# Kernel tuning notes

Hardware: AMD Instinct MI355X
Metric: run time of the kernel (lower is better)

## Reference

```python
import jax, jax.numpy as jnp
import numpy as np

N = 100000
E = 1600000
NFEAT, NHID1, NHID2, NCLASS, NSTRUC = 512, 256, 128, 40, 128


def glorot(key, shape):
    lim = 1.0 / np.sqrt(shape[0])
    return jax.random.uniform(key, shape, jnp.float32, -lim, lim)


def setup_inputs() -> dict:
    key = jax.random.key(0)
    ks = jax.random.split(key, 12)
    x = jax.random.normal(ks[0], (N, NFEAT), jnp.float32)
    edge_index = jax.random.randint(ks[1], (2, E), 0, N, jnp.int32)
    edge_weight = jax.random.uniform(ks[2], (E,), jnp.float32)
    return {
        "x": x,
        "edge_index": edge_index,
        "edge_weight": edge_weight,
        "W1": glorot(ks[3], (NFEAT, NHID1)), "b1": jnp.zeros((NHID1,), jnp.float32),
        "W2": glorot(ks[4], (NHID1, NHID2)), "b2": jnp.zeros((NHID2,), jnp.float32),
        "W3": glorot(ks[5], (NHID2, NCLASS)), "b3": jnp.zeros((NCLASS,), jnp.float32),
        "We": glorot(ks[6], (NHID1, NSTRUC)), "be": jnp.zeros((NSTRUC,), jnp.float32),
    }


def spmm(edge_index, edge_weight, support):
    # adj @ support with adj given as weighted edge list (dst <- src)
    src, dst = edge_index[0], edge_index[1]
    msgs = support[src] * edge_weight[:, None]  # [E, d]
    return jax.ops.segment_sum(msgs, dst, num_segments=N)


def gc_layer(x, edge_index, edge_weight, W, b):
    support = x @ W
    return spmm(edge_index, edge_weight, support) + b


def reference(x, edge_index, edge_weight, W1, b1, W2, b2, W3, b3, We, be):
    # eval mode: dropout is identity
    h = jax.nn.relu(gc_layer(x, edge_index, edge_weight, W1, b1))
    out1 = jax.nn.relu(gc_layer(h, edge_index, edge_weight, W2, b2))
    out1 = gc_layer(out1, edge_index, edge_weight, W3, b3)
    out2 = h @ We + be
    return jax.nn.log_softmax(out1, axis=1), out2
```

## Files before the change

kernel.cpp:

```cpp
#include <hip/hip_runtime.h>
#include <hip/hip_bf16.h>

#define NNODES 100000
#define NEDGES 1600000

typedef __attribute__((ext_vector_type(8))) short bf16x8;
typedef __attribute__((ext_vector_type(4))) short bf16x4;
typedef __attribute__((ext_vector_type(2))) short bf16x2;
typedef __attribute__((ext_vector_type(4))) float f32x4;
typedef __attribute__((ext_vector_type(2))) float f32x2;

static __device__ __forceinline__ short f2bf(float f) {
  __hip_bfloat16 b = __float2bfloat16(f);
  return __builtin_bit_cast(short, b);
}
static __device__ __forceinline__ float bf2f(short s) {
  unsigned int u = ((unsigned int)(unsigned short)s) << 16;
  return __builtin_bit_cast(float, u);
}
static __device__ __forceinline__ void fma4(f32x4& a, float w, bf16x4 v) {
  a[0] = fmaf(w, bf2f(v[0]), a[0]);
  a[1] = fmaf(w, bf2f(v[1]), a[1]);
  a[2] = fmaf(w, bf2f(v[2]), a[2]);
  a[3] = fmaf(w, bf2f(v[3]), a[3]);
}
static __device__ __forceinline__ void fma2(f32x2& a, float w, bf16x2 v) {
  a[0] = fmaf(w, bf2f(v[0]), a[0]);
  a[1] = fmaf(w, bf2f(v[1]), a[1]);
}

__global__ void wtrans_kernel(const float* __restrict__ W, short* __restrict__ Wt,
                              int K, int Nvalid, int Npad) {
  int idx = blockIdx.x * blockDim.x + threadIdx.x;
  if (idx >= Npad * K) return;
  int n = idx / K, k = idx - n * K;
  Wt[idx] = (n < Nvalid) ? f2bf(W[(size_t)k * Nvalid + n]) : (short)0;
}

__global__ void hist_kernel(const int* __restrict__ ei, int* __restrict__ deg) {
  int e = blockIdx.x * blockDim.x + threadIdx.x;
  if (e < NEDGES) atomicAdd(&deg[ei[NEDGES + e]], 1);
}

__global__ void scan1_kernel(const int* __restrict__ deg, int* __restrict__ out,
                             int* __restrict__ bsums) {
  __shared__ int lds[256];
  int tid = threadIdx.x;
  int base = blockIdx.x * 1024 + tid * 4;
  int v[4];
#pragma unroll
  for (int j = 0; j < 4; j++) v[j] = (base + j < NNODES) ? deg[base + j] : 0;
  int s = v[0] + v[1] + v[2] + v[3];
  lds[tid] = s;
  __syncthreads();
  for (int off = 1; off < 256; off <<= 1) {
    int t = (tid >= off) ? lds[tid - off] : 0;
    __syncthreads();
    lds[tid] += t;
    __syncthreads();
  }
  int incl = lds[tid];
  if (tid == 255) bsums[blockIdx.x] = incl;
  int run = incl - s;
#pragma unroll
  for (int j = 0; j < 4; j++) {
    if (base + j < NNODES) out[base + j] = run;
    run += v[j];
  }
}

__global__ void scan2_kernel(const int* __restrict__ bsums, int* __restrict__ bex, int nb) {
  __shared__ int lds[128];
  int tid = threadIdx.x;
  int s = (tid < nb) ? bsums[tid] : 0;
  lds[tid] = s;
  __syncthreads();
  for (int off = 1; off < 128; off <<= 1) {
    int t = (tid >= off) ? lds[tid - off] : 0;
    __syncthreads();
    lds[tid] += t;
    __syncthreads();
  }
  if (tid < nb) bex[tid] = lds[tid] - s;
}

__global__ void scan3_kernel(int* __restrict__ rowptr, int* __restrict__ cursor,
                             const int* __restrict__ bex) {
  int i = blockIdx.x * blockDim.x + threadIdx.x;
  if (i < NNODES) {
    int v = rowptr[i] + bex[i >> 10];
    rowptr[i] = v;
    cursor[i] = v;
  }
  if (i == 0) rowptr[NNODES] = NEDGES;
}

__global__ void scatter_kernel(const int* __restrict__ ei, const float* __restrict__ ew,
                               int* __restrict__ cursor, int2* __restrict__ edat) {
  int e = blockIdx.x * blockDim.x + threadIdx.x;
  if (e >= NEDGES) return;
  int s = ei[e], d = ei[NEDGES + e];
  int p = atomicAdd(&cursor[d], 1);
  edat[p] = make_int2(s, __float_as_int(ew[e]));
}

#define LDSTR 72
template <bool AF32, int EPI>
__launch_bounds__(256, 2)
__global__ void gemm_tiled(const void* __restrict__ Aptr, int K,
                           const short* __restrict__ Wt,
                           void* __restrict__ Cp0, float* __restrict__ Cp1,
                           const float* __restrict__ bias, int nvalid, int ldc) {
  __shared__ __align__(16) short As[128 * LDSTR];
  __shared__ __align__(16) short Bs[128 * LDSTR];
  int tid = threadIdx.x;
  int lane = tid & 63, wv = tid >> 6;
  int wr = wv >> 1, wc = wv & 1;
  int m0 = blockIdx.x * 128;
  int n0 = blockIdx.y * 128;
  f32x4 acc[4][4];
#pragma unroll
  for (int i = 0; i < 4; i++)
#pragma unroll
    for (int j = 0; j < 4; j++) acc[i][j] = (f32x4){0.f, 0.f, 0.f, 0.f};

  int srow = tid >> 3;
  int scol = (tid & 7) * 8;

  for (int k0 = 0; k0 < K; k0 += 64) {
#pragma unroll
    for (int p = 0; p < 4; p++) {
      int ml = p * 32 + srow;
      int arow = m0 + ml;
      if (arow >= NNODES) arow = NNODES - 1;
      bf16x8 av;
      if (AF32) {
        const float* ap = (const float*)Aptr + (size_t)arow * K + k0 + scol;
        f32x4 a0 = *(const f32x4*)ap;
        f32x4 a1 = *(const f32x4*)(ap + 4);
#pragma unroll
        for (int j = 0; j < 4; j++) { av[j] = f2bf(a0[j]); av[4 + j] = f2bf(a1[j]); }
      } else {
        av = *(const bf16x8*)((const short*)Aptr + (size_t)arow * K + k0 + scol);
      }
      *(bf16x8*)&As[ml * LDSTR + scol] = av;
      bf16x8 bv = *(const bf16x8*)(Wt + (size_t)(n0 + ml) * K + k0 + scol);
      *(bf16x8*)&Bs[ml * LDSTR + scol] = bv;
    }
    __syncthreads();
    int r = lane & 15, quad = lane >> 4;
#pragma unroll
    for (int kk = 0; kk < 64; kk += 32) {
      bf16x8 af[4], bfr[4];
#pragma unroll
      for (int i = 0; i < 4; i++)
        af[i] = *(const bf16x8*)&As[(wr * 64 + i * 16 + r) * LDSTR + kk + quad * 8];
#pragma unroll
      for (int j = 0; j < 4; j++)
        bfr[j] = *(const bf16x8*)&Bs[(wc * 64 + j * 16 + r) * LDSTR + kk + quad * 8];
#pragma unroll
      for (int i = 0; i < 4; i++)
#pragma unroll
        for (int j = 0; j < 4; j++)
          acc[i][j] = __builtin_amdgcn_mfma_f32_16x16x32_bf16(af[i], bfr[j], acc[i][j], 0, 0, 0);
    }
    __syncthreads();
  }

  int quad = lane >> 4, cl = lane & 15;
#pragma unroll
  for (int i = 0; i < 4; i++) {
    int rowb = m0 + wr * 64 + i * 16 + quad * 4;
#pragma unroll
    for (int rr = 0; rr < 4; rr++) {
      int row = rowb + rr;
      if (row < NNODES) {
#pragma unroll
        for (int j = 0; j < 4; j++) {
          int col = n0 + wc * 64 + j * 16 + cl;
          float v = acc[i][j][rr];
          if (EPI == 0) {
            ((short*)Cp0)[(size_t)row * ldc + col] = f2bf(v);
          } else if (EPI == 1) {
            if (col < nvalid) Cp1[(size_t)row * nvalid + col] = v;
          } else {
            if (col < 128) ((short*)Cp0)[(size_t)row * 128 + col] = f2bf(v);
            else Cp1[(size_t)row * 128 + (col - 128)] = v + bias[col - 128];
          }
        }
      }
    }
  }
}

__global__ void spmm1_kernel(const int* __restrict__ rowptr, const int2* __restrict__ edat,
                             const short* __restrict__ S,
                             const float* __restrict__ bias, short* __restrict__ H) {
  int node = blockIdx.x * 4 + (threadIdx.x >> 6);
  if (node >= NNODES) return;
  int lane = threadIdx.x & 63;
  int c0 = lane * 4;
  const short* Sc = S + c0;
  f32x4 acc0 = (f32x4){0.f, 0.f, 0.f, 0.f};
  f32x4 acc1 = (f32x4){0.f, 0.f, 0.f, 0.f};
  int beg = rowptr[node], end = rowptr[node + 1];
  int i = beg;
  for (; i + 8 <= end; i += 8) {
    int2 e[8];
    bf16x4 v[8];
#pragma unroll
    for (int j = 0; j < 8; j++) e[j] = edat[i + j];
#pragma unroll
    for (int j = 0; j < 8; j++) v[j] = *(const bf16x4*)(Sc + (size_t)e[j].x * 256);
#pragma unroll
    for (int j = 0; j < 8; j++) {
      float w = __int_as_float(e[j].y);
      if (j & 1) fma4(acc1, w, v[j]); else fma4(acc0, w, v[j]);
    }
  }
  for (; i < end; i++) {
    int2 e = edat[i];
    fma4(acc0, __int_as_float(e.y), *(const bf16x4*)(Sc + (size_t)e.x * 256));
  }
  f32x4 a;
  a[0] = acc0[0] + acc1[0]; a[1] = acc0[1] + acc1[1];
  a[2] = acc0[2] + acc1[2]; a[3] = acc0[3] + acc1[3];
  f32x4 b = *(const f32x4*)(bias + c0);
  bf16x4 h;
#pragma unroll
  for (int j = 0; j < 4; j++) h[j] = f2bf(fmaxf(a[j] + b[j], 0.f));
  *(bf16x4*)(H + (size_t)node * 256 + c0) = h;
}

__global__ void spmm2_kernel(const int* __restrict__ rowptr, const int2* __restrict__ edat,
                             const short* __restrict__ S,
                             const float* __restrict__ bias, short* __restrict__ H) {
  int node = blockIdx.x * 4 + (threadIdx.x >> 6);
  if (node >= NNODES) return;
  int lane = threadIdx.x & 63;
  int c0 = lane * 2;
  const short* Sc = S + c0;
  f32x2 acc0 = (f32x2){0.f, 0.f};
  f32x2 acc1 = (f32x2){0.f, 0.f};
  int beg = rowptr[node], end = rowptr[node + 1];
  int i = beg;
  for (; i + 8 <= end; i += 8) {
    int2 e[8];
    bf16x2 v[8];
#pragma unroll
    for (int j = 0; j < 8; j++) e[j] = edat[i + j];
#pragma unroll
    for (int j = 0; j < 8; j++) v[j] = *(const bf16x2*)(Sc + (size_t)e[j].x * 128);
#pragma unroll
    for (int j = 0; j < 8; j++) {
      float w = __int_as_float(e[j].y);
      if (j & 1) fma2(acc1, w, v[j]); else fma2(acc0, w, v[j]);
    }
  }
  for (; i < end; i++) {
    int2 e = edat[i];
    fma2(acc0, __int_as_float(e.y), *(const bf16x2*)(Sc + (size_t)e.x * 128));
  }
  float a0 = acc0[0] + acc1[0], a1 = acc0[1] + acc1[1];
  bf16x2 h;
  h[0] = f2bf(fmaxf(a0 + bias[c0 + 0], 0.f));
  h[1] = f2bf(fmaxf(a1 + bias[c0 + 1], 0.f));
  *(bf16x2*)(H + (size_t)node * 128 + c0) = h;
}

__global__ void spmm3_kernel(const int* __restrict__ rowptr, const int2* __restrict__ edat,
                             const float* __restrict__ S3,
                             const float* __restrict__ b3, float* __restrict__ out1) {
  int node = blockIdx.x * 4 + (threadIdx.x >> 6);
  if (node >= NNODES) return;
  int lane = threadIdx.x & 63;
  bool act = lane < 40;
  float acc0 = 0.f, acc1 = 0.f;
  int beg = rowptr[node], end = rowptr[node + 1];
  if (act) {
    int i = beg;
    for (; i + 8 <= end; i += 8) {
      int2 e[8];
      float v[8];
#pragma unroll
      for (int j = 0; j < 8; j++) e[j] = edat[i + j];
#pragma unroll
      for (int j = 0; j < 8; j++) v[j] = S3[(size_t)e[j].x * 40 + lane];
#pragma unroll
      for (int j = 0; j < 8; j++) {
        float w = __int_as_float(e[j].y);
        if (j & 1) acc1 = fmaf(w, v[j], acc1); else acc0 = fmaf(w, v[j], acc0);
      }
    }
    for (; i < end; i++) {
      int2 e = edat[i];
      acc0 = fmaf(__int_as_float(e.y), S3[(size_t)e.x * 40 + lane], acc0);
    }
  }
  float acc = acc0 + acc1;
  if (act) acc += b3[lane];
  float v = act ? acc : -__builtin_inff();
  for (int off = 32; off > 0; off >>= 1) v = fmaxf(v, __shfl_xor(v, off));
  float e = act ? expf(acc - v) : 0.f;
  for (int off = 32; off > 0; off >>= 1) e += __shfl_xor(e, off);
  float ls = logf(e);
  if (act) out1[(size_t)node * 40 + lane] = acc - v - ls;
}

extern "C" void kernel_launch(void* const* d_in, const int* in_sizes, int n_in,
                              void* d_out, int out_size, void* d_ws, size_t ws_size,
                              hipStream_t stream) {
  const float* x  = (const float*)d_in[0];
  const int*   ei = (const int*)d_in[1];
  const float* ew = (const float*)d_in[2];
  const float* W1 = (const float*)d_in[3];
  const float* b1 = (const float*)d_in[4];
  const float* W2 = (const float*)d_in[5];
  const float* b2 = (const float*)d_in[6];
  const float* W3 = (const float*)d_in[7];
  const float* b3 = (const float*)d_in[8];
  const float* We = (const float*)d_in[9];
  const float* be = (const float*)d_in[10];
  float* out1 = (float*)d_out;
  float* out2 = (float*)d_out + (size_t)NNODES * 40;

  char* w = (char*)d_ws;
  size_t off = 0;
  auto alloc = [&](size_t bytes) -> char* {
    char* p = w + off;
    off += (bytes + 255) & ~(size_t)255;
    return p;
  };
  int*   deg    = (int*)alloc((size_t)NNODES * 4);
  int*   rowptr = (int*)alloc((size_t)(NNODES + 1) * 4);
  int*   cursor = (int*)alloc((size_t)NNODES * 4);
  int*   bsums  = (int*)alloc(512);
  int*   bex    = (int*)alloc(512);
  int2*  edat   = (int2*)alloc((size_t)NEDGES * 8);
  short* Wt1    = (short*)alloc((size_t)256 * 512 * 2);
  short* Wt2e   = (short*)alloc((size_t)256 * 256 * 2);
  short* Wt3    = (short*)alloc((size_t)128 * 128 * 2);
  short* S1bf   = (short*)alloc((size_t)NNODES * 256 * 2);
  short* Hbf    = (short*)alloc((size_t)NNODES * 256 * 2);
  short* S2bf   = (short*)alloc((size_t)NNODES * 128 * 2);
  short* Tbf    = (short*)alloc((size_t)NNODES * 128 * 2);
  float* S3     = (float*)alloc((size_t)NNODES * 40 * 4);

  hipMemsetAsync(deg, 0, (size_t)NNODES * 4, stream);
  hist_kernel<<<(NEDGES + 255) / 256, 256, 0, stream>>>(ei, deg);
  int nb = (NNODES + 1023) / 1024;
  scan1_kernel<<<nb, 256, 0, stream>>>(deg, rowptr, bsums);
  scan2_kernel<<<1, 128, 0, stream>>>(bsums, bex, nb);
  scan3_kernel<<<(NNODES + 255) / 256, 256, 0, stream>>>(rowptr, cursor, bex);
  scatter_kernel<<<(NEDGES + 255) / 256, 256, 0, stream>>>(ei, ew, cursor, edat);

  wtrans_kernel<<<(256 * 512 + 255) / 256, 256, 0, stream>>>(W1, Wt1, 512, 256, 256);
  wtrans_kernel<<<(128 * 256 + 255) / 256, 256, 0, stream>>>(W2, Wt2e, 256, 128, 128);
  wtrans_kernel<<<(128 * 256 + 255) / 256, 256, 0, stream>>>(We, Wt2e + (size_t)128 * 256, 256, 128, 128);
  wtrans_kernel<<<(128 * 128 + 255) / 256, 256, 0, stream>>>(W3, Wt3, 128, 40, 128);

  int gblocks = (NNODES + 127) / 128;
  int sblocks = (NNODES + 3) / 4;

  gemm_tiled<true, 0><<<dim3(gblocks, 2), 256, 0, stream>>>(x, 512, Wt1, S1bf, nullptr, nullptr, 256, 256);
  spmm1_kernel<<<sblocks, 256, 0, stream>>>(rowptr, edat, S1bf, b1, Hbf);
  gemm_tiled<false, 2><<<dim3(gblocks, 2), 256, 0, stream>>>(Hbf, 256, Wt2e, S2bf, out2, be, 256, 128);
  spmm2_kernel<<<sblocks, 256, 0, stream>>>(rowptr, edat, S2bf, b2, Tbf);
  gemm_tiled<false, 1><<<dim3(gblocks, 1), 256, 0, stream>>>(Tbf, 128, Wt3, nullptr, S3, nullptr, 40, 40);
  spmm3_kernel<<<sblocks, 256, 0, stream>>>(rowptr, edat, S3, b3, out1);
}
```

Baseline: 884.5 us.

## Build CSR via two-level bucket sort and swap GEMM grid axes

Replaces the per-node histogram, three-kernel scan and atomic scatter with a two-pass bucketed counting sort. Edges are first grouped into 128-node buckets using LDS histograms, then each bucket is sorted locally in LDS, which writes rowptr and edat. This cuts global atomics and should make the edge writes closer to coalesced. It packs the local destination into the high bits of the source index, which assumes node ids fit in 17 bits, and reuses the S3 buffer as scratch. Separately, the GEMM grid axes are swapped so the N-tiles of one M-row block run next to each other, which should improve L2 reuse of the A rows.

```diff
diff --git a/kernel.cpp b/kernel.cpp
--- a/kernel.cpp
+++ b/kernel.cpp
@@ -3,6 +3,8 @@
 
 #define NNODES 100000
 #define NEDGES 1600000
+#define BSH 7
+#define NBUCK ((NNODES + 127) >> 7)
 
 typedef __attribute__((ext_vector_type(8))) short bf16x8;
 typedef __attribute__((ext_vector_type(4))) short bf16x4;
@@ -37,71 +39,99 @@
   Wt[idx] = (n < Nvalid) ? f2bf(W[(size_t)k * Nvalid + n]) : (short)0;
 }
 
-__global__ void hist_kernel(const int* __restrict__ ei, int* __restrict__ deg) {
-  int e = blockIdx.x * blockDim.x + threadIdx.x;
-  if (e < NEDGES) atomicAdd(&deg[ei[NEDGES + e]], 1);
-}
-
-__global__ void scan1_kernel(const int* __restrict__ deg, int* __restrict__ out,
-                             int* __restrict__ bsums) {
-  __shared__ int lds[256];
+__global__ void bcount_kernel(const int* __restrict__ ei, int* __restrict__ bcnt) {
+  __shared__ int h[NBUCK];
+  for (int i = threadIdx.x; i < NBUCK; i += 256) h[i] = 0;
+  __syncthreads();
+  int stride = gridDim.x * 256;
+  for (int e = blockIdx.x * 256 + threadIdx.x; e < NEDGES; e += stride)
+    atomicAdd(&h[ei[NEDGES + e] >> BSH], 1);
+  __syncthreads();
+  for (int i = threadIdx.x; i < NBUCK; i += 256)
+    if (h[i]) atomicAdd(&bcnt[i], h[i]);
+}
+
+__global__ void bscan_kernel(const int* __restrict__ bcnt, int* __restrict__ bbase,
+                             int* __restrict__ bcur, int* __restrict__ rowptr) {
+  __shared__ int lds[1024];
+  int t = threadIdx.x;
+  int c = (t < NBUCK) ? bcnt[t] : 0;
+  lds[t] = c;
+  __syncthreads();
+  for (int off = 1; off < 1024; off <<= 1) {
+    int v = (t >= off) ? lds[t - off] : 0;
+    __syncthreads();
+    lds[t] += v;
+    __syncthreads();
+  }
+  if (t < NBUCK) {
+    int ex = lds[t] - c;
+    bbase[t] = ex;
+    bcur[t] = ex;
+  }
+  if (t == NBUCK) bbase[t] = NEDGES;
+  if (t == 0) rowptr[NNODES] = NEDGES;
+}
+
+#define P4CHUNK 8192
+__global__ void bscatter_kernel(const int* __restrict__ ei, const float* __restrict__ ew,
+                                int* __restrict__ bcur, int2* __restrict__ tmp) {
+  __shared__ int cnt[NBUCK];
+  __shared__ int pos[NBUCK];
   int tid = threadIdx.x;
-  int base = blockIdx.x * 1024 + tid * 4;
-  int v[4];
-#pragma unroll
-  for (int j = 0; j < 4; j++) v[j] = (base + j < NNODES) ? deg[base + j] : 0;
-  int s = v[0] + v[1] + v[2] + v[3];
-  lds[tid] = s;
-  __syncthreads();
-  for (int off = 1; off < 256; off <<= 1) {
-    int t = (tid >= off) ? lds[tid - off] : 0;
-    __syncthreads();
-    lds[tid] += t;
-    __syncthreads();
-  }
-  int incl = lds[tid];
-  if (tid == 255) bsums[blockIdx.x] = incl;
-  int run = incl - s;
-#pragma unroll
-  for (int j = 0; j < 4; j++) {
-    if (base + j < NNODES) out[base + j] = run;
-    run += v[j];
-  }
-}
-
-__global__ void scan2_kernel(const int* __restrict__ bsums, int* __restrict__ bex, int nb) {
-  __shared__ int lds[128];
+  for (int i = tid; i < NBUCK; i += 256) cnt[i] = 0;
+  __syncthreads();
+  int base = blockIdx.x * P4CHUNK;
+  int end = base + P4CHUNK;
+  if (end > NEDGES) end = NEDGES;
+  for (int e = base + tid; e < end; e += 256)
+    atomicAdd(&cnt[ei[NEDGES + e] >> BSH], 1);
+  __syncthreads();
+  for (int i = tid; i < NBUCK; i += 256)
+    if (cnt[i]) pos[i] = atomicAdd(&bcur[i], cnt[i]);
+  __syncthreads();
+  for (int e = base + tid; e < end; e += 256) {
+    int d = ei[NEDGES + e];
+    int b = d >> BSH;
+    int p = atomicAdd(&pos[b], 1);
+    tmp[p] = make_int2(ei[e] | ((d & 127) << 17), __float_as_int(ew[e]));
+  }
+}
+
+__global__ void bsort_kernel(const int* __restrict__ bbase, const int2* __restrict__ tmp,
+                             int2* __restrict__ edat, int* __restrict__ rowptr) {
+  __shared__ int hist[128];
+  __shared__ int cur[128];
+  int b = blockIdx.x;
   int tid = threadIdx.x;
-  int s = (tid < nb) ? bsums[tid] : 0;
-  lds[tid] = s;
+  int base = bbase[b], cnt = bbase[b + 1] - base;
+  if (tid < 128) hist[tid] = 0;
+  __syncthreads();
+  for (int i = tid; i < cnt; i += 256)
+    atomicAdd(&hist[(tmp[base + i].x >> 17) & 127], 1);
+  __syncthreads();
+  int c = (tid < 128) ? hist[tid] : 0;
+  if (tid < 128) cur[tid] = c;
   __syncthreads();
   for (int off = 1; off < 128; off <<= 1) {
-    int t = (tid >= off) ? lds[tid - off] : 0;
-    __syncthreads();
-    lds[tid] += t;
-    __syncthreads();
-  }
-  if (tid < nb) bex[tid] = lds[tid] - s;
-}
-
-__global__ void scan3_kernel(int* __restrict__ rowptr, int* __restrict__ cursor,
-                             const int* __restrict__ bex) {
-  int i = blockIdx.x * blockDim.x + threadIdx.x;
-  if (i < NNODES) {
-    int v = rowptr[i] + bex[i >> 10];
-    rowptr[i] = v;
-    cursor[i] = v;
-  }
-  if (i == 0) rowptr[NNODES] = NEDGES;
-}
-
-__global__ void scatter_kernel(const int* __restrict__ ei, const float* __restrict__ ew,
-                               int* __restrict__ cursor, int2* __restrict__ edat) {
-  int e = blockIdx.x * blockDim.x + threadIdx.x;
-  if (e >= NEDGES) return;
-  int s = ei[e], d = ei[NEDGES + e];
-  int p = atomicAdd(&cursor[d], 1);
-  edat[p] = make_int2(s, __float_as_int(ew[e]));
+    int v = (tid < 128 && tid >= off) ? cur[tid - off] : 0;
+    __syncthreads();
+    if (tid < 128) cur[tid] += v;
+    __syncthreads();
+  }
+  if (tid < 128) {
+    int ex = cur[tid] - c;
+    int node = (b << BSH) + tid;
+    if (node < NNODES) rowptr[node] = base + ex;
+    cur[tid] = base + ex;
+  }
+  __syncthreads();
+  for (int i = tid; i < cnt; i += 256) {
+    int2 r = tmp[base + i];
+    int d = (r.x >> 17) & 127;
+    int p = atomicAdd(&cur[d], 1);
+    edat[p] = make_int2(r.x & 0x1FFFF, r.y);
+  }
 }
 
 #define LDSTR 72
@@ -116,8 +146,8 @@
   int tid = threadIdx.x;
   int lane = tid & 63, wv = tid >> 6;
   int wr = wv >> 1, wc = wv & 1;
-  int m0 = blockIdx.x * 128;
-  int n0 = blockIdx.y * 128;
+  int m0 = blockIdx.y * 128;
+  int n0 = blockIdx.x * 128;
   f32x4 acc[4][4];
 #pragma unroll
   for (int i = 0; i < 4; i++)
@@ -331,11 +361,10 @@
     off += (bytes + 255) & ~(size_t)255;
     return p;
   };
-  int*   deg    = (int*)alloc((size_t)NNODES * 4);
   int*   rowptr = (int*)alloc((size_t)(NNODES + 1) * 4);
-  int*   cursor = (int*)alloc((size_t)NNODES * 4);
-  int*   bsums  = (int*)alloc(512);
-  int*   bex    = (int*)alloc(512);
+  int*   bcnt   = (int*)alloc((size_t)NBUCK * 4);
+  int*   bbase  = (int*)alloc((size_t)(NBUCK + 1) * 4);
+  int*   bcur   = (int*)alloc((size_t)NBUCK * 4);
   int2*  edat   = (int2*)alloc((size_t)NEDGES * 8);
   short* Wt1    = (short*)alloc((size_t)256 * 512 * 2);
   short* Wt2e   = (short*)alloc((size_t)256 * 256 * 2);
@@ -345,14 +374,13 @@
   short* S2bf   = (short*)alloc((size_t)NNODES * 128 * 2);
   short* Tbf    = (short*)alloc((size_t)NNODES * 128 * 2);
   float* S3     = (float*)alloc((size_t)NNODES * 40 * 4);
-
-  hipMemsetAsync(deg, 0, (size_t)NNODES * 4, stream);
-  hist_kernel<<<(NEDGES + 255) / 256, 256, 0, stream>>>(ei, deg);
-  int nb = (NNODES + 1023) / 1024;
-  scan1_kernel<<<nb, 256, 0, stream>>>(deg, rowptr, bsums);
-  scan2_kernel<<<1, 128, 0, stream>>>(bsums, bex, nb);
-  scan3_kernel<<<(NNODES + 255) / 256, 256, 0, stream>>>(rowptr, cursor, bex);
-  scatter_kernel<<<(NEDGES + 255) / 256, 256, 0, stream>>>(ei, ew, cursor, edat);
+  int2*  tmp    = (int2*)S3;
+
+  hipMemsetAsync(bcnt, 0, (size_t)NBUCK * 4, stream);
+  bcount_kernel<<<256, 256, 0, stream>>>(ei, bcnt);
+  bscan_kernel<<<1, 1024, 0, stream>>>(bcnt, bbase, bcur, rowptr);
+  bscatter_kernel<<<(NEDGES + P4CHUNK - 1) / P4CHUNK, 256, 0, stream>>>(ei, ew, bcur, tmp);
+  bsort_kernel<<<NBUCK, 256, 0, stream>>>(bbase, tmp, edat, rowptr);
 
   wtrans_kernel<<<(256 * 512 + 255) / 256, 256, 0, stream>>>(W1, Wt1, 512, 256, 256);
   wtrans_kernel<<<(128 * 256 + 255) / 256, 256, 0, stream>>>(W2, Wt2e, 256, 128, 128);
@@ -362,10 +390,10 @@
   int gblocks = (NNODES + 127) / 128;
   int sblocks = (NNODES + 3) / 4;
 
-  gemm_tiled<true, 0><<<dim3(gblocks, 2), 256, 0, stream>>>(x, 512, Wt1, S1bf, nullptr, nullptr, 256, 256);
+  gemm_tiled<true, 0><<<dim3(2, gblocks), 256, 0, stream>>>(x, 512, Wt1, S1bf, nullptr, nullptr, 256, 256);
   spmm1_kernel<<<sblocks, 256, 0, stream>>>(rowptr, edat, S1bf, b1, Hbf);
-  gemm_tiled<false, 2><<<dim3(gblocks, 2), 256, 0, stream>>>(Hbf, 256, Wt2e, S2bf, out2, be, 256, 128);
+  gemm_tiled<false, 2><<<dim3(2, gblocks), 256, 0, stream>>>(Hbf, 256, Wt2e, S2bf, out2, be, 256, 128);
   spmm2_kernel<<<sblocks, 256, 0, stream>>>(rowptr, edat, S2bf, b2, Tbf);
-  gemm_tiled<false, 1><<<dim3(gblocks, 1), 256, 0, stream>>>(Tbf, 128, Wt3, nullptr, S3, nullptr, 40, 40);
+  gemm_tiled<false, 1><<<dim3(1, gblocks), 256, 0, stream>>>(Tbf, 128, Wt3, nullptr, S3, nullptr, 40, 40);
   spmm3_kernel<<<sblocks, 256, 0, stream>>>(rowptr, edat, S3, b3, out1);
 }
```

Measured after the change: 789.0 us. -10.8%, faster.
